# Optimization experiments

Hardware: AMD Instinct MI355X
Metric: run time of the kernel (lower is better)

Reference implementation:

```python
import jax, jax.numpy as jnp
import numpy as np

N_NODES = 50000
NEG_SLOPE = 0.2


def setup_inputs() -> dict:
    key = jax.random.key(0)
    k1, k2, k3, k4 = jax.random.split(key, 4)
    N, E, F, H, C = 50000, 800000, 128, 4, 32
    x = jax.random.normal(k1, (N, F), dtype=jnp.float32)
    edge_index = jax.random.randint(k2, (2, E), 0, N, dtype=jnp.int32)
    weight = jax.random.normal(k3, (F, H * C), dtype=jnp.float32) * 0.1  # glorot-ish scale
    att = jax.random.normal(k4, (1, H, 2 * C), dtype=jnp.float32) * 0.1
    bias = jnp.zeros((C,), dtype=jnp.float32)
    return {"x": x, "edge_index": edge_index, "weight": weight, "att": att, "bias": bias}


def reference(x, edge_index, weight, att, bias):
    N = x.shape[0]
    H, C2 = att.shape[1], att.shape[2]
    C = C2 // 2
    # linear projection -> [N, H, C]
    xw = jnp.matmul(x, weight).reshape(N, H, C)
    row, col = edge_index[0], edge_index[1]
    # per-edge attention logits: gather both endpoints, concat along channel
    x_i = xw[row]                     # [E, H, C]
    x_j = xw[col]                     # [E, H, C]
    cat_x = jnp.concatenate([x_i, x_j], axis=-1)      # [E, H, 2C]
    alpha = jnp.sum(cat_x * att, axis=-1)             # [E, H]
    alpha = jnp.where(alpha >= 0, alpha, NEG_SLOPE * alpha)  # leaky_relu
    # segment softmax grouped by row (source index, as in the torch code)
    seg_max = jax.ops.segment_max(alpha, row, num_segments=N)
    seg_max = jnp.where(jnp.isfinite(seg_max), seg_max, 0.0)
    alpha = jnp.exp(alpha - seg_max[row])
    seg_sum = jax.ops.segment_sum(alpha, row, num_segments=N)
    alpha = alpha / (seg_sum[row] + 1e-16)            # [E, H]
    # PyG propagate: message = alpha * x_j where x_j = x[edge_index[0]],
    # aggregated (scatter-add) into target = edge_index[1]
    msg = alpha[..., None] * xw[row]                  # [E, H, C]
    out = jax.ops.segment_sum(msg, col, num_segments=N)  # [N, H, C]
    out = out.mean(axis=1) + bias                     # concat=False -> head mean, + bias
    return out
```

## Files before the change

### kernel.cpp

```cpp
#include <hip/hip_runtime.h>
#include <hip/hip_fp16.h>

#define FDIM 128
#define HEADS 4
#define CD 32
#define BM 64

typedef __attribute__((ext_vector_type(8))) short bfrag;
typedef __attribute__((ext_vector_type(4))) float ffrag;

static __device__ __forceinline__ unsigned short f2bf(float v) {
    unsigned u = __float_as_uint(v);
    u += 0x7FFF + ((u >> 16) & 1);
    return (unsigned short)(u >> 16);
}
static __device__ __forceinline__ float bf2f(unsigned short u) {
    return __uint_as_float(((unsigned)u) << 16);
}

__global__ __launch_bounds__(256) void k_wsplit(const float* __restrict__ w,
                                                unsigned short* __restrict__ wt_hi,
                                                unsigned short* __restrict__ wt_lo)
{
    int i = blockIdx.x * 256 + threadIdx.x;
    float v = w[i];
    unsigned short h = f2bf(v);
    float r = v - bf2f(h);
    int k = i >> 7, n = i & 127;
    wt_hi[n * FDIM + k] = h;
    wt_lo[n * FDIM + k] = f2bf(r);
}

__global__ __launch_bounds__(256) void k_gemm(const float* __restrict__ x,
                                              const unsigned short* __restrict__ wt_hi,
                                              const unsigned short* __restrict__ wt_lo,
                                              const float* __restrict__ att,
                                              unsigned short* __restrict__ xwh,
                                              float* __restrict__ a_src,
                                              float* __restrict__ a_dst,
                                              float4* __restrict__ zero_base,
                                              int nz4, int N)
{
    __shared__ float accs[BM * 132];
    __shared__ float attl[HEADS * 2 * CD];
    int t = threadIdx.x;
    int row0 = blockIdx.x * BM;
    for (int i = blockIdx.x * 256 + t; i < nz4; i += gridDim.x * 256)
        zero_base[i] = make_float4(0.f, 0.f, 0.f, 0.f);
    attl[t] = att[t];

    int l = t & 63, wv = t >> 6;
    int la = l & 15, lr = l >> 4;
    int arow = row0 + wv * 16 + la;
    bool aval = arow < N;
    const float* xbase = x + (size_t)arow * FDIM + lr * 8;

    ffrag acc[8] = {};
#pragma unroll
    for (int ks = 0; ks < 4; ks++) {
        float xv[8] = {0.f, 0.f, 0.f, 0.f, 0.f, 0.f, 0.f, 0.f};
        if (aval) {
            float4 f0 = *(const float4*)(xbase + ks * 32);
            float4 f1 = *(const float4*)(xbase + ks * 32 + 4);
            xv[0] = f0.x; xv[1] = f0.y; xv[2] = f0.z; xv[3] = f0.w;
            xv[4] = f1.x; xv[5] = f1.y; xv[6] = f1.z; xv[7] = f1.w;
        }
        bfrag ah, al;
#pragma unroll
        for (int j = 0; j < 8; j++) {
            unsigned short h = f2bf(xv[j]);
            ah[j] = (short)h;
            al[j] = (short)f2bf(xv[j] - bf2f(h));
        }
        int boff = ks * 32 + lr * 8;
#pragma unroll
        for (int ct = 0; ct < 8; ct++) {
            int o = (ct * 16 + la) * FDIM + boff;
            bfrag bh = *(const bfrag*)(wt_hi + o);
            bfrag bl = *(const bfrag*)(wt_lo + o);
            acc[ct] = __builtin_amdgcn_mfma_f32_16x16x32_bf16(ah, bh, acc[ct], 0, 0, 0);
            acc[ct] = __builtin_amdgcn_mfma_f32_16x16x32_bf16(ah, bl, acc[ct], 0, 0, 0);
            acc[ct] = __builtin_amdgcn_mfma_f32_16x16x32_bf16(al, bh, acc[ct], 0, 0, 0);
        }
    }

#pragma unroll
    for (int i = 0; i < 4; i++) {
        int r = row0 + wv * 16 + lr * 4 + i;
        if (r < N) {
            uint2 pa, pb;
            pa.x = (unsigned)f2bf(acc[0][i]) | ((unsigned)f2bf(acc[2][i]) << 16);
            pa.y = (unsigned)f2bf(acc[4][i]) | ((unsigned)f2bf(acc[6][i]) << 16);
            pb.x = (unsigned)f2bf(acc[1][i]) | ((unsigned)f2bf(acc[3][i]) << 16);
            pb.y = (unsigned)f2bf(acc[5][i]) | ((unsigned)f2bf(acc[7][i]) << 16);
            *(uint2*)&xwh[(size_t)r * FDIM + la * 4] = pa;
            *(uint2*)&xwh[(size_t)r * FDIM + 64 + la * 4] = pb;
        }
    }
#pragma unroll
    for (int ct = 0; ct < 8; ct++)
#pragma unroll
        for (int i = 0; i < 4; i++)
            accs[(wv * 16 + lr * 4 + i) * 132 + ct * 16 + la] = acc[ct][i];
    __syncthreads();
    int row = t >> 2, h = t & 3;
    const float* ap = &attl[h * 2 * CD];
    const float* xr = &accs[row * 132 + h * CD];
    float s = 0.f, d = 0.f;
#pragma unroll 8
    for (int c = 0; c < CD; c++) { float v = xr[c]; s += v * ap[c]; d += v * ap[CD + c]; }
    int n = row0 + row;
    if (n < N) { a_src[n * 4 + h] = s; a_dst[n * 4 + h] = d; }
}

__global__ __launch_bounds__(256) void k_esum(const int* __restrict__ ei, int E,
                                              const float* __restrict__ a_src,
                                              const float* __restrict__ a_dst,
                                              float* __restrict__ seg,
                                              __half* __restrict__ ealpha)
{
    int gid = blockIdx.x * 256 + threadIdx.x;
    if (gid >= E * HEADS) return;
    int e = gid >> 2, h = gid & 3;
    int r = ei[e], cl = ei[E + e];
    float a = a_src[r * 4 + h] + a_dst[cl * 4 + h];
    a = a >= 0.f ? a : 0.2f * a;
    float ex = __expf(a);
    ealpha[gid] = __float2half(ex);
    atomicAdd(&seg[r * 4 + h], ex);
}

__global__ __launch_bounds__(256) void k_scatter(const int* __restrict__ ei, int E,
                                                 const __half* __restrict__ ealpha,
                                                 const float* __restrict__ seg,
                                                 const unsigned short* __restrict__ xwh,
                                                 __half2* __restrict__ out_acc2)
{
    int t = threadIdx.x;
    int le = t >> 4, c2 = t & 15;
    int e = blockIdx.x * 16 + le;
    if (e >= E) return;
    int r = ei[e], cl = ei[E + e];
    int lane = t & 63;
    float av = 0.f;
    if (c2 < 4) av = 0.25f * __half2float(ealpha[e * 4 + c2]) / (seg[r * 4 + c2] + 1e-16f);
    uint4 q = ((const uint4*)(xwh + (size_t)r * FDIM))[c2];
    float a0 = __shfl(av, (lane & 48) + 0, 64);
    float a1 = __shfl(av, (lane & 48) + 1, 64);
    float a2 = __shfl(av, (lane & 48) + 2, 64);
    float a3 = __shfl(av, (lane & 48) + 3, 64);
    float v0 = a0 * bf2f((unsigned short)(q.x & 0xFFFF)) + a1 * bf2f((unsigned short)(q.x >> 16))
             + a2 * bf2f((unsigned short)(q.y & 0xFFFF)) + a3 * bf2f((unsigned short)(q.y >> 16));
    float v1 = a0 * bf2f((unsigned short)(q.z & 0xFFFF)) + a1 * bf2f((unsigned short)(q.z >> 16))
             + a2 * bf2f((unsigned short)(q.w & 0xFFFF)) + a3 * bf2f((unsigned short)(q.w >> 16));
    unsafeAtomicAdd(&out_acc2[(size_t)cl * 16 + c2], __floats2half2_rn(v0, v1));
}

__global__ void k_final(const __half2* __restrict__ out_acc2, const float4* __restrict__ bias,
                        float4* __restrict__ out, int N)
{
    int i = blockIdx.x * 256 + threadIdx.x;
    if (i >= N * 8) return;
    float4 b = bias[i & 7];
    float2 f0 = __half22float2(out_acc2[i * 2]);
    float2 f1 = __half22float2(out_acc2[i * 2 + 1]);
    out[i] = make_float4(f0.x + b.x, f0.y + b.y, f1.x + b.z, f1.y + b.w);
}

extern "C" void kernel_launch(void* const* d_in, const int* in_sizes, int n_in,
                              void* d_out, int out_size, void* d_ws, size_t ws_size,
                              hipStream_t stream)
{
    const float* x    = (const float*)d_in[0];
    const int*   ei   = (const int*)d_in[1];
    const float* w    = (const float*)d_in[2];
    const float* att  = (const float*)d_in[3];
    const float* bias = (const float*)d_in[4];
    float* out = (float*)d_out;
    int N = in_sizes[0] / FDIM;
    int E = in_sizes[1] / 2;

    unsigned short* xwh = (unsigned short*)d_ws;
    float* fws      = (float*)(xwh + (size_t)N * FDIM);
    float* a_src    = fws;
    float* a_dst    = a_src + (size_t)N * HEADS;
    float* seg      = a_dst + (size_t)N * HEADS;
    __half2* out_acc2 = (__half2*)(seg + (size_t)N * HEADS);
    __half* ealpha  = (__half*)(out_acc2 + (size_t)N * 16);
    unsigned short* wt_hi = (unsigned short*)(ealpha + (size_t)E * HEADS);
    unsigned short* wt_lo = wt_hi + FDIM * FDIM;

    int nz4 = N * 5;

    k_wsplit<<<(FDIM * FDIM) / 256, 256, 0, stream>>>(w, wt_hi, wt_lo);
    k_gemm<<<(N + BM - 1) / BM, 256, 0, stream>>>(x, wt_hi, wt_lo, att, xwh, a_src, a_dst,
                                                  (float4*)seg, nz4, N);
    k_esum<<<(E * HEADS + 255) / 256, 256, 0, stream>>>(ei, E, a_src, a_dst, seg, ealpha);
    k_scatter<<<(E + 15) / 16, 256, 0, stream>>>(ei, E, ealpha, seg, xwh, out_acc2);
    k_final<<<(N * 8 + 255) / 256, 256, 0, stream>>>(out_acc2, (const float4*)bias, (float4*)out, N);
}
```

Measured before the change: 210.0 us.

## Bucket edges by source range so scatter reads xw rows with better locality

Adds a histogram and scan that split edges into 8 buckets by source node range. The edge-score kernel now handles all four heads per thread with vectorised loads, and writes packed records (row, col, half alphas) into bucket order. The scatter kernel processes one bucket per block group, which narrows the xw gather working set for better L2 reuse, and reads packed records instead of separate index and alpha arrays. The cost is two extra small kernels, more atomics in the edge kernel, and a 16-byte-per-edge record buffer.

```diff
diff --git a/kernel.cpp b/kernel.cpp
--- a/kernel.cpp
+++ b/kernel.cpp
@@ -5,6 +5,7 @@
 #define HEADS 4
 #define CD 32
 #define BM 64
+#define NB 8
 
 typedef __attribute__((ext_vector_type(8))) short bfrag;
 typedef __attribute__((ext_vector_type(4))) float ffrag;
@@ -20,15 +21,39 @@
 
 __global__ __launch_bounds__(256) void k_wsplit(const float* __restrict__ w,
                                                 unsigned short* __restrict__ wt_hi,
-                                                unsigned short* __restrict__ wt_lo)
+                                                unsigned short* __restrict__ wt_lo,
+                                                int* __restrict__ meta)
 {
     int i = blockIdx.x * 256 + threadIdx.x;
+    if (i < 32) meta[i] = 0;
     float v = w[i];
     unsigned short h = f2bf(v);
     float r = v - bf2f(h);
     int k = i >> 7, n = i & 127;
     wt_hi[n * FDIM + k] = h;
     wt_lo[n * FDIM + k] = f2bf(r);
+}
+
+__global__ __launch_bounds__(256) void k_hist(const int* __restrict__ ei, int E, int N,
+                                              int* __restrict__ meta)
+{
+    __shared__ int h[NB];
+    int t = threadIdx.x;
+    if (t < NB) h[t] = 0;
+    __syncthreads();
+    for (int e = blockIdx.x * 256 + t; e < E; e += gridDim.x * 256)
+        atomicAdd(&h[(ei[e] * NB) / N], 1);
+    __syncthreads();
+    if (t < NB) atomicAdd(&meta[t], h[t]);
+}
+
+__global__ void k_scan8(int* __restrict__ meta)
+{
+    if (threadIdx.x == 0) {
+        int s = 0;
+        for (int b = 0; b < NB; b++) { int c = meta[b]; meta[8 + b] = s; meta[17 + b] = s; s += c; }
+        meta[16] = s;
+    }
 }
 
 __global__ __launch_bounds__(256) void k_gemm(const float* __restrict__ x,
@@ -113,47 +138,82 @@
     if (n < N) { a_src[n * 4 + h] = s; a_dst[n * 4 + h] = d; }
 }
 
-__global__ __launch_bounds__(256) void k_esum(const int* __restrict__ ei, int E,
+__global__ __launch_bounds__(256) void k_esum(const int* __restrict__ ei, int E, int N,
                                               const float* __restrict__ a_src,
                                               const float* __restrict__ a_dst,
                                               float* __restrict__ seg,
-                                              __half* __restrict__ ealpha)
-{
-    int gid = blockIdx.x * 256 + threadIdx.x;
-    if (gid >= E * HEADS) return;
-    int e = gid >> 2, h = gid & 3;
-    int r = ei[e], cl = ei[E + e];
-    float a = a_src[r * 4 + h] + a_dst[cl * 4 + h];
-    a = a >= 0.f ? a : 0.2f * a;
-    float ex = __expf(a);
-    ealpha[gid] = __float2half(ex);
-    atomicAdd(&seg[r * 4 + h], ex);
-}
-
-__global__ __launch_bounds__(256) void k_scatter(const int* __restrict__ ei, int E,
-                                                 const __half* __restrict__ ealpha,
+                                              int* __restrict__ meta,
+                                              uint4* __restrict__ recs)
+{
+    __shared__ int lcnt[NB];
+    __shared__ int gbase[NB];
+    int t = threadIdx.x;
+    if (t < NB) lcnt[t] = 0;
+    __syncthreads();
+    int e = blockIdx.x * 256 + t;
+    bool v = e < E;
+    int r = 0, cl = 0, b = 0, loc = 0;
+    unsigned a01 = 0, a23 = 0;
+    if (v) {
+        r = ei[e]; cl = ei[E + e];
+        float4 as = *(const float4*)&a_src[r * 4];
+        float4 ad = *(const float4*)&a_dst[cl * 4];
+        float x0 = as.x + ad.x; x0 = x0 >= 0.f ? x0 : 0.2f * x0;
+        float x1 = as.y + ad.y; x1 = x1 >= 0.f ? x1 : 0.2f * x1;
+        float x2 = as.z + ad.z; x2 = x2 >= 0.f ? x2 : 0.2f * x2;
+        float x3 = as.w + ad.w; x3 = x3 >= 0.f ? x3 : 0.2f * x3;
+        float e0 = __expf(x0), e1 = __expf(x1), e2 = __expf(x2), e3 = __expf(x3);
+        atomicAdd(&seg[r * 4 + 0], e0);
+        atomicAdd(&seg[r * 4 + 1], e1);
+        atomicAdd(&seg[r * 4 + 2], e2);
+        atomicAdd(&seg[r * 4 + 3], e3);
+        __half2 p01 = __floats2half2_rn(e0, e1);
+        __half2 p23 = __floats2half2_rn(e2, e3);
+        a01 = *(unsigned*)&p01;
+        a23 = *(unsigned*)&p23;
+        b = (r * NB) / N;
+        loc = atomicAdd(&lcnt[b], 1);
+    }
+    __syncthreads();
+    if (t < NB && lcnt[t] > 0) gbase[t] = atomicAdd(&meta[17 + t], lcnt[t]);
+    __syncthreads();
+    if (v) recs[gbase[b] + loc] = make_uint4((unsigned)r, (unsigned)cl, a01, a23);
+}
+
+__global__ __launch_bounds__(256) void k_scatter(const uint4* __restrict__ recs,
+                                                 const int* __restrict__ meta,
                                                  const float* __restrict__ seg,
                                                  const unsigned short* __restrict__ xwh,
-                                                 __half2* __restrict__ out_acc2)
-{
-    int t = threadIdx.x;
-    int le = t >> 4, c2 = t & 15;
-    int e = blockIdx.x * 16 + le;
-    if (e >= E) return;
-    int r = ei[e], cl = ei[E + e];
-    int lane = t & 63;
-    float av = 0.f;
-    if (c2 < 4) av = 0.25f * __half2float(ealpha[e * 4 + c2]) / (seg[r * 4 + c2] + 1e-16f);
-    uint4 q = ((const uint4*)(xwh + (size_t)r * FDIM))[c2];
-    float a0 = __shfl(av, (lane & 48) + 0, 64);
-    float a1 = __shfl(av, (lane & 48) + 1, 64);
-    float a2 = __shfl(av, (lane & 48) + 2, 64);
-    float a3 = __shfl(av, (lane & 48) + 3, 64);
-    float v0 = a0 * bf2f((unsigned short)(q.x & 0xFFFF)) + a1 * bf2f((unsigned short)(q.x >> 16))
-             + a2 * bf2f((unsigned short)(q.y & 0xFFFF)) + a3 * bf2f((unsigned short)(q.y >> 16));
-    float v1 = a0 * bf2f((unsigned short)(q.z & 0xFFFF)) + a1 * bf2f((unsigned short)(q.z >> 16))
-             + a2 * bf2f((unsigned short)(q.w & 0xFFFF)) + a3 * bf2f((unsigned short)(q.w >> 16));
-    unsafeAtomicAdd(&out_acc2[(size_t)cl * 16 + c2], __floats2half2_rn(v0, v1));
+                                                 __half2* __restrict__ out_acc2, int bpb)
+{
+    int t = threadIdx.x;
+    int le = t >> 4, c2 = t & 15, lane = t & 63;
+    int b = blockIdx.x & 7;
+    int lo = meta[8 + b], hi = meta[9 + b];
+    int cnt = hi - lo;
+    for (int chunk = blockIdx.x >> 3; chunk * 16 < cnt; chunk += bpb) {
+        int idx = lo + chunk * 16 + le;
+        bool v = idx < hi;
+        uint4 rec = recs[v ? idx : lo];
+        int r = (int)rec.x, cl = (int)rec.y;
+        float av = 0.f;
+        if (v && c2 < 4) {
+            unsigned az = (c2 < 2) ? rec.z : rec.w;
+            __half2 hh = *(__half2*)&az;
+            float a = (c2 & 1) ? __high2float(hh) : __low2float(hh);
+            av = 0.25f * a / (seg[r * 4 + c2] + 1e-16f);
+        }
+        uint4 q = ((const uint4*)(xwh + (size_t)r * FDIM))[c2];
+        float a0 = __shfl(av, (lane & 48) + 0, 64);
+        float a1 = __shfl(av, (lane & 48) + 1, 64);
+        float a2 = __shfl(av, (lane & 48) + 2, 64);
+        float a3 = __shfl(av, (lane & 48) + 3, 64);
+        float v0 = a0 * bf2f((unsigned short)(q.x & 0xFFFF)) + a1 * bf2f((unsigned short)(q.x >> 16))
+                 + a2 * bf2f((unsigned short)(q.y & 0xFFFF)) + a3 * bf2f((unsigned short)(q.y >> 16));
+        float v1 = a0 * bf2f((unsigned short)(q.z & 0xFFFF)) + a1 * bf2f((unsigned short)(q.z >> 16))
+                 + a2 * bf2f((unsigned short)(q.w & 0xFFFF)) + a3 * bf2f((unsigned short)(q.w >> 16));
+        if (v) unsafeAtomicAdd(&out_acc2[(size_t)cl * 16 + c2], __floats2half2_rn(v0, v1));
+    }
 }
 
 __global__ void k_final(const __half2* __restrict__ out_acc2, const float4* __restrict__ bias,
@@ -181,21 +241,24 @@
     int E = in_sizes[1] / 2;
 
     unsigned short* xwh = (unsigned short*)d_ws;
-    float* fws      = (float*)(xwh + (size_t)N * FDIM);
-    float* a_src    = fws;
+    float* a_src    = (float*)(xwh + (size_t)N * FDIM);
     float* a_dst    = a_src + (size_t)N * HEADS;
     float* seg      = a_dst + (size_t)N * HEADS;
     __half2* out_acc2 = (__half2*)(seg + (size_t)N * HEADS);
-    __half* ealpha  = (__half*)(out_acc2 + (size_t)N * 16);
-    unsigned short* wt_hi = (unsigned short*)(ealpha + (size_t)E * HEADS);
+    unsigned short* wt_hi = (unsigned short*)(out_acc2 + (size_t)N * 16);
     unsigned short* wt_lo = wt_hi + FDIM * FDIM;
+    int* meta = (int*)(wt_lo + FDIM * FDIM);
+    uint4* recs = (uint4*)(meta + 32);
 
     int nz4 = N * 5;
-
-    k_wsplit<<<(FDIM * FDIM) / 256, 256, 0, stream>>>(w, wt_hi, wt_lo);
+    int bpb = (E / NB + E / 32 + 15) / 16;
+
+    k_wsplit<<<(FDIM * FDIM) / 256, 256, 0, stream>>>(w, wt_hi, wt_lo, meta);
+    k_hist<<<512, 256, 0, stream>>>(ei, E, N, meta);
+    k_scan8<<<1, 64, 0, stream>>>(meta);
     k_gemm<<<(N + BM - 1) / BM, 256, 0, stream>>>(x, wt_hi, wt_lo, att, xwh, a_src, a_dst,
                                                   (float4*)seg, nz4, N);
-    k_esum<<<(E * HEADS + 255) / 256, 256, 0, stream>>>(ei, E, a_src, a_dst, seg, ealpha);
-    k_scatter<<<(E + 15) / 16, 256, 0, stream>>>(ei, E, ealpha, seg, xwh, out_acc2);
+    k_esum<<<(E + 255) / 256, 256, 0, stream>>>(ei, E, N, a_src, a_dst, seg, meta, recs);
+    k_scatter<<<NB * bpb, 256, 0, stream>>>(recs, meta, seg, xwh, out_acc2, bpb);
     k_final<<<(N * 8 + 255) / 256, 256, 0, stream>>>(out_acc2, (const float4*)bias, (float4*)out, N);
 }
```

New measurement: 351.7 us. +67.5%, slower.

## Bucket edges by source row so scatter blocks gather XCD-local rows

Applied to the files above, without the earlier changes.

Adds a histogram, scan and stable-ish bucketing pass that groups edges into 8 buckets by source row range and packs row, col and alpha into 16-byte records. The scatter kernel then assigns blocks to buckets by block index modulo 8, so each group of blocks gathers only a slice of the projected features, aiming for better L2 cache locality per die. It adds extra kernels and a full read/write of edge records, which may outweigh the locality gain.

```diff
diff --git a/kernel.cpp b/kernel.cpp
--- a/kernel.cpp
+++ b/kernel.cpp
@@ -5,6 +5,8 @@
 #define HEADS 4
 #define CD 32
 #define BM 64
+#define NB 8
+#define CHUNK 1024
 
 typedef __attribute__((ext_vector_type(8))) short bfrag;
 typedef __attribute__((ext_vector_type(4))) float ffrag;
@@ -29,6 +31,48 @@
     int k = i >> 7, n = i & 127;
     wt_hi[n * FDIM + k] = h;
     wt_lo[n * FDIM + k] = f2bf(r);
+}
+
+__global__ __launch_bounds__(256) void k_hist(const int* __restrict__ ei, int E, int N,
+                                              int* __restrict__ cntT, int nblk)
+{
+    __shared__ int h[NB];
+    int t = threadIdx.x;
+    if (t < NB) h[t] = 0;
+    __syncthreads();
+    int base = blockIdx.x * CHUNK;
+#pragma unroll
+    for (int i = 0; i < CHUNK / 256; i++) {
+        int e = base + i * 256 + t;
+        if (e < E) atomicAdd(&h[(ei[e] * NB) / N], 1);
+    }
+    __syncthreads();
+    if (t < NB) cntT[t * nblk + blockIdx.x] = h[t];
+}
+
+__global__ __launch_bounds__(512) void k_scan(const int* __restrict__ cntT,
+                                              int* __restrict__ prefT,
+                                              int* __restrict__ meta, int nblk)
+{
+    __shared__ int tot[NB];
+    int t = threadIdx.x, w = t >> 6, lane = t & 63;
+    int carry = 0;
+    for (int c0 = 0; c0 < nblk; c0 += 64) {
+        int i = c0 + lane;
+        int v = (i < nblk) ? cntT[w * nblk + i] : 0;
+        int x = v;
+#pragma unroll
+        for (int d = 1; d < 64; d <<= 1) { int y = __shfl_up(x, d, 64); if (lane >= d) x += y; }
+        if (i < nblk) prefT[w * nblk + i] = carry + x - v;
+        carry += __shfl(x, 63, 64);
+    }
+    if (lane == 0) tot[w] = carry;
+    __syncthreads();
+    if (t == 0) {
+        int s = 0;
+        for (int b = 0; b < NB; b++) { meta[8 + b] = s; s += tot[b]; }
+        meta[16] = s;
+    }
 }
 
 __global__ __launch_bounds__(256) void k_gemm(const float* __restrict__ x,
@@ -130,30 +174,65 @@
     atomicAdd(&seg[r * 4 + h], ex);
 }
 
-__global__ __launch_bounds__(256) void k_scatter(const int* __restrict__ ei, int E,
+__global__ __launch_bounds__(256) void k_sortrec(const int* __restrict__ ei, int E, int N,
                                                  const __half* __restrict__ ealpha,
+                                                 const int* __restrict__ prefT,
+                                                 const int* __restrict__ meta,
+                                                 uint4* __restrict__ recs, int nblk)
+{
+    __shared__ int lcnt[NB];
+    __shared__ int boff[NB];
+    int t = threadIdx.x, blk = blockIdx.x;
+    if (t < NB) { lcnt[t] = 0; boff[t] = meta[8 + t] + prefT[t * nblk + blk]; }
+    __syncthreads();
+    int base = blk * CHUNK;
+#pragma unroll
+    for (int i = 0; i < CHUNK / 256; i++) {
+        int e = base + i * 256 + t;
+        if (e < E) {
+            int r = ei[e], cl = ei[E + e];
+            uint2 a = *(const uint2*)(ealpha + (size_t)e * 4);
+            int b = (r * NB) / N;
+            int loc = atomicAdd(&lcnt[b], 1);
+            recs[boff[b] + loc] = make_uint4((unsigned)r, (unsigned)cl, a.x, a.y);
+        }
+    }
+}
+
+__global__ __launch_bounds__(256) void k_scatter(const uint4* __restrict__ recs,
+                                                 const int* __restrict__ meta,
                                                  const float* __restrict__ seg,
                                                  const unsigned short* __restrict__ xwh,
-                                                 __half2* __restrict__ out_acc2)
+                                                 __half2* __restrict__ out_acc2, int bpb)
 {
     int t = threadIdx.x;
-    int le = t >> 4, c2 = t & 15;
-    int e = blockIdx.x * 16 + le;
-    if (e >= E) return;
-    int r = ei[e], cl = ei[E + e];
-    int lane = t & 63;
-    float av = 0.f;
-    if (c2 < 4) av = 0.25f * __half2float(ealpha[e * 4 + c2]) / (seg[r * 4 + c2] + 1e-16f);
-    uint4 q = ((const uint4*)(xwh + (size_t)r * FDIM))[c2];
-    float a0 = __shfl(av, (lane & 48) + 0, 64);
-    float a1 = __shfl(av, (lane & 48) + 1, 64);
-    float a2 = __shfl(av, (lane & 48) + 2, 64);
-    float a3 = __shfl(av, (lane & 48) + 3, 64);
-    float v0 = a0 * bf2f((unsigned short)(q.x & 0xFFFF)) + a1 * bf2f((unsigned short)(q.x >> 16))
-             + a2 * bf2f((unsigned short)(q.y & 0xFFFF)) + a3 * bf2f((unsigned short)(q.y >> 16));
-    float v1 = a0 * bf2f((unsigned short)(q.z & 0xFFFF)) + a1 * bf2f((unsigned short)(q.z >> 16))
-             + a2 * bf2f((unsigned short)(q.w & 0xFFFF)) + a3 * bf2f((unsigned short)(q.w >> 16));
-    unsafeAtomicAdd(&out_acc2[(size_t)cl * 16 + c2], __floats2half2_rn(v0, v1));
+    int le = t >> 4, c2 = t & 15, lane = t & 63;
+    int b = blockIdx.x & 7;
+    int lo = meta[8 + b], hi = meta[9 + b];
+    int cnt = hi - lo;
+    for (int chunk = blockIdx.x >> 3; chunk * 16 < cnt; chunk += bpb) {
+        int idx = lo + chunk * 16 + le;
+        bool v = idx < hi;
+        uint4 rec = recs[v ? idx : lo];
+        int r = (int)rec.x, cl = (int)rec.y;
+        float av = 0.f;
+        if (v && c2 < 4) {
+            unsigned az = (c2 < 2) ? rec.z : rec.w;
+            __half2 hh = *(__half2*)&az;
+            float a = (c2 & 1) ? __high2float(hh) : __low2float(hh);
+            av = 0.25f * a / (seg[r * 4 + c2] + 1e-16f);
+        }
+        uint4 q = ((const uint4*)(xwh + (size_t)r * FDIM))[c2];
+        float a0 = __shfl(av, (lane & 48) + 0, 64);
+        float a1 = __shfl(av, (lane & 48) + 1, 64);
+        float a2 = __shfl(av, (lane & 48) + 2, 64);
+        float a3 = __shfl(av, (lane & 48) + 3, 64);
+        float v0 = a0 * bf2f((unsigned short)(q.x & 0xFFFF)) + a1 * bf2f((unsigned short)(q.x >> 16))
+                 + a2 * bf2f((unsigned short)(q.y & 0xFFFF)) + a3 * bf2f((unsigned short)(q.y >> 16));
+        float v1 = a0 * bf2f((unsigned short)(q.z & 0xFFFF)) + a1 * bf2f((unsigned short)(q.z >> 16))
+                 + a2 * bf2f((unsigned short)(q.w & 0xFFFF)) + a3 * bf2f((unsigned short)(q.w >> 16));
+        if (v) unsafeAtomicAdd(&out_acc2[(size_t)cl * 16 + c2], __floats2half2_rn(v0, v1));
+    }
 }
 
 __global__ void k_final(const __half2* __restrict__ out_acc2, const float4* __restrict__ bias,
@@ -179,23 +258,31 @@
     float* out = (float*)d_out;
     int N = in_sizes[0] / FDIM;
     int E = in_sizes[1] / 2;
+    int nblk = (E + CHUNK - 1) / CHUNK;
 
     unsigned short* xwh = (unsigned short*)d_ws;
-    float* fws      = (float*)(xwh + (size_t)N * FDIM);
-    float* a_src    = fws;
+    float* a_src    = (float*)(xwh + (size_t)N * FDIM);
     float* a_dst    = a_src + (size_t)N * HEADS;
     float* seg      = a_dst + (size_t)N * HEADS;
     __half2* out_acc2 = (__half2*)(seg + (size_t)N * HEADS);
-    __half* ealpha  = (__half*)(out_acc2 + (size_t)N * 16);
+    uint4* recs     = (uint4*)(out_acc2 + (size_t)N * 16);
+    __half* ealpha  = (__half*)(recs + (size_t)E);
     unsigned short* wt_hi = (unsigned short*)(ealpha + (size_t)E * HEADS);
     unsigned short* wt_lo = wt_hi + FDIM * FDIM;
+    int* meta = (int*)(wt_lo + FDIM * FDIM);
+    int* cntT = meta + 32;
+    int* prefT = cntT + NB * nblk;
 
     int nz4 = N * 5;
+    int bpb = (E / NB + E / 32 + 15) / 16;
 
     k_wsplit<<<(FDIM * FDIM) / 256, 256, 0, stream>>>(w, wt_hi, wt_lo);
+    k_hist<<<nblk, 256, 0, stream>>>(ei, E, N, cntT, nblk);
+    k_scan<<<1, 512, 0, stream>>>(cntT, prefT, meta, nblk);
     k_gemm<<<(N + BM - 1) / BM, 256, 0, stream>>>(x, wt_hi, wt_lo, att, xwh, a_src, a_dst,
                                                   (float4*)seg, nz4, N);
     k_esum<<<(E * HEADS + 255) / 256, 256, 0, stream>>>(ei, E, a_src, a_dst, seg, ealpha);
-    k_scatter<<<(E + 15) / 16, 256, 0, stream>>>(ei, E, ealpha, seg, xwh, out_acc2);
+    k_sortrec<<<nblk, 256, 0, stream>>>(ei, E, N, ealpha, prefT, meta, recs, nblk);
+    k_scatter<<<NB * bpb, 256, 0, stream>>>(recs, meta, seg, xwh, out_acc2, bpb);
     k_final<<<(N * 8 + 255) / 256, 256, 0, stream>>>(out_acc2, (const float4*)bias, (float4*)out, N);
 }
```

Measured after the change: 227.1 us. +8.2%, slower.

## Replace atomic edge scatter with counting-sort CSR build and per-node gather aggregation

Applied to the files above, without the earlier changes.

Per-edge half2 atomic adds into an fp16 output accumulator are replaced by a destination-grouped layout. In-degree counts are taken in k_esum, a single-block scan produces offsets, and each edge's normalized attention and source index are placed into a 16-byte record. A per-node kernel then gathers the source features and accumulates in fp32, writing the output with bias directly, which removes the separate final kernel and the accumulator zeroing. The gain in atomic traffic is traded for an extra serial scan kernel, a cursor atomic per edge and random record writes.

```diff
diff --git a/kernel.cpp b/kernel.cpp
--- a/kernel.cpp
+++ b/kernel.cpp
@@ -117,6 +117,7 @@
                                               const float* __restrict__ a_src,
                                               const float* __restrict__ a_dst,
                                               float* __restrict__ seg,
+                                              int* __restrict__ cnt,
                                               __half* __restrict__ ealpha)
 {
     int gid = blockIdx.x * 256 + threadIdx.x;
@@ -128,43 +129,79 @@
     float ex = __expf(a);
     ealpha[gid] = __float2half(ex);
     atomicAdd(&seg[r * 4 + h], ex);
-}
-
-__global__ __launch_bounds__(256) void k_scatter(const int* __restrict__ ei, int E,
-                                                 const __half* __restrict__ ealpha,
-                                                 const float* __restrict__ seg,
-                                                 const unsigned short* __restrict__ xwh,
-                                                 __half2* __restrict__ out_acc2)
-{
-    int t = threadIdx.x;
-    int le = t >> 4, c2 = t & 15;
-    int e = blockIdx.x * 16 + le;
+    if (h == 0) atomicAdd(&cnt[cl], 1);
+}
+
+__global__ __launch_bounds__(1024) void k_scanN(const int* __restrict__ cnt,
+                                                int* __restrict__ base,
+                                                int* __restrict__ cursor, int N, int E)
+{
+    __shared__ int wsum[16];
+    int t = threadIdx.x, lane = t & 63, w = t >> 6;
+    int span = (N + 1023) / 1024;
+    int s0 = t * span, s1 = min(s0 + span, N);
+    int sum = 0;
+    for (int i = s0; i < s1; i++) sum += cnt[i];
+    int x = sum;
+#pragma unroll
+    for (int d = 1; d < 64; d <<= 1) { int y = __shfl_up(x, d, 64); if (lane >= d) x += y; }
+    if (lane == 63) wsum[w] = x;
+    __syncthreads();
+    int woff = 0;
+    for (int i = 0; i < w; i++) woff += wsum[i];
+    int run = woff + x - sum;
+    for (int i = s0; i < s1; i++) { base[i] = run; cursor[i] = run; run += cnt[i]; }
+    if (t == 1023) base[N] = E;
+}
+
+__global__ __launch_bounds__(256) void k_place(const int* __restrict__ ei, int E,
+                                               const __half* __restrict__ ealpha,
+                                               const float* __restrict__ seg,
+                                               int* __restrict__ cursor,
+                                               uint4* __restrict__ recs)
+{
+    int e = blockIdx.x * 256 + threadIdx.x;
     if (e >= E) return;
     int r = ei[e], cl = ei[E + e];
-    int lane = t & 63;
-    float av = 0.f;
-    if (c2 < 4) av = 0.25f * __half2float(ealpha[e * 4 + c2]) / (seg[r * 4 + c2] + 1e-16f);
-    uint4 q = ((const uint4*)(xwh + (size_t)r * FDIM))[c2];
-    float a0 = __shfl(av, (lane & 48) + 0, 64);
-    float a1 = __shfl(av, (lane & 48) + 1, 64);
-    float a2 = __shfl(av, (lane & 48) + 2, 64);
-    float a3 = __shfl(av, (lane & 48) + 3, 64);
-    float v0 = a0 * bf2f((unsigned short)(q.x & 0xFFFF)) + a1 * bf2f((unsigned short)(q.x >> 16))
-             + a2 * bf2f((unsigned short)(q.y & 0xFFFF)) + a3 * bf2f((unsigned short)(q.y >> 16));
-    float v1 = a0 * bf2f((unsigned short)(q.z & 0xFFFF)) + a1 * bf2f((unsigned short)(q.z >> 16))
-             + a2 * bf2f((unsigned short)(q.w & 0xFFFF)) + a3 * bf2f((unsigned short)(q.w >> 16));
-    unsafeAtomicAdd(&out_acc2[(size_t)cl * 16 + c2], __floats2half2_rn(v0, v1));
-}
-
-__global__ void k_final(const __half2* __restrict__ out_acc2, const float4* __restrict__ bias,
-                        float4* __restrict__ out, int N)
-{
-    int i = blockIdx.x * 256 + threadIdx.x;
-    if (i >= N * 8) return;
-    float4 b = bias[i & 7];
-    float2 f0 = __half22float2(out_acc2[i * 2]);
-    float2 f1 = __half22float2(out_acc2[i * 2 + 1]);
-    out[i] = make_float4(f0.x + b.x, f0.y + b.y, f1.x + b.z, f1.y + b.w);
+    uint2 a = *(const uint2*)(ealpha + (size_t)e * 4);
+    __half2 e01 = *(__half2*)&a.x, e23 = *(__half2*)&a.y;
+    float4 s4 = *(const float4*)&seg[r * 4];
+    float na0 = 0.25f * __low2float(e01) / (s4.x + 1e-16f);
+    float na1 = 0.25f * __high2float(e01) / (s4.y + 1e-16f);
+    float na2 = 0.25f * __low2float(e23) / (s4.z + 1e-16f);
+    float na3 = 0.25f * __high2float(e23) / (s4.w + 1e-16f);
+    __half2 n01 = __floats2half2_rn(na0, na1), n23 = __floats2half2_rn(na2, na3);
+    int pos = atomicAdd(&cursor[cl], 1);
+    recs[pos] = make_uint4((unsigned)r, *(unsigned*)&n01, *(unsigned*)&n23, 0u);
+}
+
+__global__ __launch_bounds__(256) void k_aggregate(const uint4* __restrict__ recs,
+                                                   const int* __restrict__ base,
+                                                   const unsigned short* __restrict__ xwh,
+                                                   const float* __restrict__ bias,
+                                                   float* __restrict__ out, int N)
+{
+    int t = threadIdx.x;
+    int ln = t >> 4, c2 = t & 15;
+    int cl = blockIdx.x * 16 + ln;
+    if (cl >= N) return;
+    int lo = base[cl], hi = base[cl + 1];
+    float acc0 = 0.f, acc1 = 0.f;
+    for (int i = lo; i < hi; i++) {
+        uint4 rec = recs[i];
+        int r = (int)rec.x;
+        __half2 h01 = *(__half2*)&rec.y;
+        __half2 h23 = *(__half2*)&rec.z;
+        float na0 = __low2float(h01), na1 = __high2float(h01);
+        float na2 = __low2float(h23), na3 = __high2float(h23);
+        uint4 q = ((const uint4*)(xwh + (size_t)r * FDIM))[c2];
+        acc0 += na0 * bf2f((unsigned short)(q.x & 0xFFFF)) + na1 * bf2f((unsigned short)(q.x >> 16))
+              + na2 * bf2f((unsigned short)(q.y & 0xFFFF)) + na3 * bf2f((unsigned short)(q.y >> 16));
+        acc1 += na0 * bf2f((unsigned short)(q.z & 0xFFFF)) + na1 * bf2f((unsigned short)(q.z >> 16))
+              + na2 * bf2f((unsigned short)(q.w & 0xFFFF)) + na3 * bf2f((unsigned short)(q.w >> 16));
+    }
+    float2 b = ((const float2*)bias)[c2];
+    ((float2*)out)[(size_t)cl * 16 + c2] = make_float2(acc0 + b.x, acc1 + b.y);
 }
 
 extern "C" void kernel_launch(void* const* d_in, const int* in_sizes, int n_in,
@@ -181,21 +218,24 @@
     int E = in_sizes[1] / 2;
 
     unsigned short* xwh = (unsigned short*)d_ws;
-    float* fws      = (float*)(xwh + (size_t)N * FDIM);
-    float* a_src    = fws;
+    uint4* recs     = (uint4*)(xwh + (size_t)N * FDIM);
+    __half* ealpha  = (__half*)(recs + (size_t)E);
+    float* a_src    = (float*)(ealpha + (size_t)E * HEADS);
     float* a_dst    = a_src + (size_t)N * HEADS;
     float* seg      = a_dst + (size_t)N * HEADS;
-    __half2* out_acc2 = (__half2*)(seg + (size_t)N * HEADS);
-    __half* ealpha  = (__half*)(out_acc2 + (size_t)N * 16);
-    unsigned short* wt_hi = (unsigned short*)(ealpha + (size_t)E * HEADS);
+    int*   cnt      = (int*)(seg + (size_t)N * HEADS);
+    int*   base     = cnt + N + 4;
+    int*   cursor   = base + N + 4;
+    unsigned short* wt_hi = (unsigned short*)(cursor + N + 4);
     unsigned short* wt_lo = wt_hi + FDIM * FDIM;
 
-    int nz4 = N * 5;
+    int nz4 = (N * 5 + 19) / 4;
 
     k_wsplit<<<(FDIM * FDIM) / 256, 256, 0, stream>>>(w, wt_hi, wt_lo);
     k_gemm<<<(N + BM - 1) / BM, 256, 0, stream>>>(x, wt_hi, wt_lo, att, xwh, a_src, a_dst,
                                                   (float4*)seg, nz4, N);
-    k_esum<<<(E * HEADS + 255) / 256, 256, 0, stream>>>(ei, E, a_src, a_dst, seg, ealpha);
-    k_scatter<<<(E + 15) / 16, 256, 0, stream>>>(ei, E, ealpha, seg, xwh, out_acc2);
-    k_final<<<(N * 8 + 255) / 256, 256, 0, stream>>>(out_acc2, (const float4*)bias, (float4*)out, N);
-}
+    k_esum<<<(E * HEADS + 255) / 256, 256, 0, stream>>>(ei, E, a_src, a_dst, seg, cnt, ealpha);
+    k_scanN<<<1, 1024, 0, stream>>>(cnt, base, cursor, N, E);
+    k_place<<<(E + 255) / 256, 256, 0, stream>>>(ei, E, ealpha, seg, cursor, recs);
+    k_aggregate<<<(N + 15) / 16, 256, 0, stream>>>(recs, base, xwh, bias, out, N);
+}
```

Result: slower. 375.8 us (+79.0%).
